# Optimization experiments

Hardware: AMD Instinct MI355X
Metric: run time of the kernel (lower is better)

Reference implementation:

```python
import jax, jax.numpy as jnp
import numpy as np
import math

B, S, D, H = 4, 2048, 768, 12
HD = D // H  # 64


def setup_inputs() -> dict:
    key = jax.random.key(0)
    ks = jax.random.split(key, 9)
    s = 0.02
    return {
        "hidden_states": jax.random.normal(ks[0], (B, S, D), jnp.float32),
        "layout_q": jax.random.normal(ks[1], (B, S, D), jnp.float32),
        "layout_k": jax.random.normal(ks[2], (B, S, D), jnp.float32),
        "attention_mask": jnp.zeros((B, 1, 1, S), jnp.float32),
        "Wq": jax.random.normal(ks[3], (D, D), jnp.float32) * s,
        "bq": jnp.zeros((D,), jnp.float32),
        "Wk": jax.random.normal(ks[4], (D, D), jnp.float32) * s,
        "bk": jnp.zeros((D,), jnp.float32),
        "Wv": jax.random.normal(ks[5], (D, D), jnp.float32) * s,
        "bv": jnp.zeros((D,), jnp.float32),
    }


def _split_heads(x):
    # [B,S,D] -> [B,H,S,HD]
    return x.reshape(B, S, H, HD).transpose(0, 2, 1, 3)


def reference(hidden_states, layout_q, layout_k, attention_mask, Wq, bq, Wk, bk, Wv, bv):
    q = _split_heads(hidden_states @ Wq.T + bq)
    k = _split_heads(hidden_states @ Wk.T + bk)
    v = _split_heads(hidden_states @ Wv.T + bv)
    lq = _split_heads(layout_q)
    lk = _split_heads(layout_k)
    scale = 1.0 / math.sqrt(HD)
    # dual-stream scores: content + layout, both [B,H,S,S]
    scores = (jnp.einsum("bhqd,bhkd->bhqk", q, k)
              + jnp.einsum("bhqd,bhkd->bhqk", lq, lk)) * scale
    scores = scores + attention_mask
    probs = jax.nn.softmax(scores, axis=-1)
    ctx = jnp.einsum("bhqk,bhkd->bhqd", probs, v)
    return ctx.transpose(0, 2, 1, 3).reshape(B, S, D)
```

## Files before the change

kernel.cpp:

```cpp
#include <hip/hip_runtime.h>


typedef __attribute__((ext_vector_type(8))) short short8;
typedef __attribute__((ext_vector_type(4))) float floatx4;

#define LOG2E 1.4426950408889634f
#define QSCL 0.18033688011112042f

static constexpr int Sn = 2048, Dn = 768, Hn = 12, BHn = 48;

__device__ __forceinline__ unsigned short f2bf(float f) {
  unsigned u = __float_as_uint(f);
  u += 0x7FFFu + ((u >> 16) & 1u);
  return (unsigned short)(u >> 16);
}

typedef const __attribute__((address_space(1))) unsigned int* gas_t;
typedef __attribute__((address_space(3))) unsigned int* las_t;
__device__ __forceinline__ void async16(const void* g, void* l) {
  __builtin_amdgcn_global_load_lds((gas_t)g, (las_t)l, 16, 0, 0);
}

__global__ void cast_hs_kernel(const float* __restrict__ in, unsigned short* __restrict__ out, int n4) {
  int i = blockIdx.x * 256 + threadIdx.x;
  if (i >= n4) return;
  float4 v = ((const float4*)in)[i];
  ushort4 o = make_ushort4(f2bf(v.x), f2bf(v.y), f2bf(v.z), f2bf(v.w));
  ((ushort4*)out)[i] = o;
}

__global__ void cast_w_kernel(const float* __restrict__ w0, const float* __restrict__ w1,
                              const float* __restrict__ w2, unsigned short* __restrict__ out) {
  int i = blockIdx.x * 256 + threadIdx.x;
  const float* src = (blockIdx.y == 0) ? w0 : (blockIdx.y == 1) ? w1 : w2;
  float4 v = ((const float4*)src)[i];
  ushort4 o = make_ushort4(f2bf(v.x), f2bf(v.y), f2bf(v.z), f2bf(v.w));
  ((ushort4*)(out + (size_t)blockIdx.y * Dn * Dn))[i] = o;
}

__global__ void pack_layout_kernel(const float* __restrict__ lq, const float* __restrict__ lk,
                                   unsigned short* __restrict__ Qc, unsigned short* __restrict__ Kc) {
  int idx = blockIdx.x * 256 + threadIdx.x;
  const float* src = blockIdx.y ? lk : lq;
  unsigned short* dst = blockIdx.y ? Kc : Qc;
  const float sc = blockIdx.y ? 1.0f : QSCL;
  int d4 = idx & 15;
  int t = idx >> 4;
  int h = t % Hn;
  int bs = t / Hn;
  int b = bs >> 11, s = bs & (Sn - 1);
  float4 v = ((const float4*)src)[idx];
  ushort4 o = make_ushort4(f2bf(v.x * sc), f2bf(v.y * sc), f2bf(v.z * sc), f2bf(v.w * sc));
  size_t off = ((size_t)(b * Hn + h) * Sn + s) * 128 + 64 + d4 * 4;
  *(ushort4*)(dst + off) = o;
}

__global__ __launch_bounds__(256, 2)
void proj_kernel(const unsigned short* __restrict__ X,
                 const unsigned short* __restrict__ Wb,
                 const float* __restrict__ bq, const float* __restrict__ bk, const float* __restrict__ bv,
                 unsigned short* __restrict__ Qc, unsigned short* __restrict__ Kc,
                 unsigned short* __restrict__ Vt) {
  __shared__ __align__(16) unsigned short sMem[16384];
  unsigned short* const sA = sMem;
  unsigned short* const sB = sMem + 8192;

  const int z = blockIdx.z;
  const unsigned short* W = Wb + (size_t)z * Dn * Dn;
  const float* bias = (z == 0) ? bq : (z == 1) ? bk : bv;

  const int t = threadIdx.x;
  const int lane = t & 63, wave = t >> 6;
  const int wm = wave >> 1, wn = wave & 1;
  const int quad = lane >> 4, col15 = lane & 15;
  const int m0 = blockIdx.y * 128, n0 = blockIdx.x * 128;

  const int srow = lane >> 3, schunk = lane & 7;

  floatx4 acc[4][4];
#pragma unroll
  for (int i = 0; i < 4; i++)
#pragma unroll
    for (int j = 0; j < 4; j++) acc[i][j] = (floatx4){0.f, 0.f, 0.f, 0.f};

  for (int k0 = 0; k0 < Dn; k0 += 64) {
    __syncthreads();
#pragma unroll
    for (int c = 0; c < 4; c++) {
      int row = wave * 32 + c * 8 + srow;
      int g = schunk ^ (row & 7);
      async16(X + (size_t)(m0 + row) * Dn + k0 + g * 8, sA + (wave * 32 + c * 8) * 64);
      async16(W + (size_t)(n0 + row) * Dn + k0 + g * 8, sB + (wave * 32 + c * 8) * 64);
    }
    __syncthreads();
#pragma unroll
    for (int kk = 0; kk < 2; kk++) {
      short8 af[4], bf[4];
      const int slot = ((kk * 4 + quad) ^ (col15 & 7)) * 8;
#pragma unroll
      for (int i = 0; i < 4; i++)
        af[i] = *(const short8*)(sA + (wm * 64 + i * 16 + col15) * 64 + slot);
#pragma unroll
      for (int j = 0; j < 4; j++)
        bf[j] = *(const short8*)(sB + (wn * 64 + j * 16 + col15) * 64 + slot);
#pragma unroll
      for (int i = 0; i < 4; i++)
#pragma unroll
        for (int j = 0; j < 4; j++)
          acc[i][j] = __builtin_amdgcn_mfma_f32_16x16x32_bf16(af[i], bf[j], acc[i][j], 0, 0, 0);
    }
  }

  __syncthreads();
  const int b = m0 >> 11;
  const int s0g = m0 & (Sn - 1);
  const int h0 = n0 >> 6;

  if (z < 2) {
    const float scl = (z == 0) ? QSCL : 1.0f;
    unsigned short* dst0 = (z == 0) ? Qc : Kc;
#pragma unroll
    for (int j = 0; j < 4; j++) {
      int nl = wn * 64 + j * 16 + col15;
      float bias_n = bias[n0 + nl];
#pragma unroll
      for (int i = 0; i < 4; i++) {
        int mb = wm * 64 + i * 16 + quad * 4;
#pragma unroll
        for (int r = 0; r < 4; r++) {
          int m = mb + r;
          sMem[m * 128 + (nl ^ (((m >> 2) & 3) << 4))] = f2bf((acc[i][j][r] + bias_n) * scl);
        }
      }
    }
    __syncthreads();
#pragma unroll
    for (int cc = 0; cc < 8; cc++) {
      int idx = cc * 256 + t;
      int m = idx >> 4, piece = idx & 15;
      int h = h0 + (piece >> 3), d8 = piece & 7;
      short8 v = *(const short8*)(sMem + m * 128 + (piece ^ (((m >> 2) & 3) << 1)) * 8);
      *(short8*)(dst0 + ((size_t)(b * Hn + h) * Sn + s0g + m) * 128 + d8 * 8) = v;
    }
  } else {
#pragma unroll
    for (int j = 0; j < 4; j++) {
      int nl = wn * 64 + j * 16 + col15;
      float bias_n = bias[n0 + nl];
#pragma unroll
      for (int i = 0; i < 4; i++) {
        int mb = wm * 64 + i * 16 + quad * 4;
        ushort4 pk = make_ushort4(f2bf(acc[i][j][0] + bias_n), f2bf(acc[i][j][1] + bias_n),
                                  f2bf(acc[i][j][2] + bias_n), f2bf(acc[i][j][3] + bias_n));
        *(ushort4*)(sMem + nl * 128 + (mb ^ ((nl & 7) << 4))) = pk;
      }
    }
    __syncthreads();
#pragma unroll
    for (int cc = 0; cc < 8; cc++) {
      int idx = cc * 256 + t;
      int nl = idx >> 4, piece = idx & 15;
      int h = h0 + (nl >> 6), d = nl & 63;
      short8 v = *(const short8*)(sMem + nl * 128 + (piece ^ ((nl & 7) << 1)) * 8);
      *(short8*)(Vt + ((size_t)(b * Hn + h) * 64 + d) * Sn + s0g + piece * 8) = v;
    }
  }
}

__global__ __launch_bounds__(256, 3)
void attn_kernel(const unsigned short* __restrict__ Qc,
                 const unsigned short* __restrict__ Kc,
                 const unsigned short* __restrict__ Vt,
                 const float* __restrict__ mask,
                 float* __restrict__ out) {
  constexpr int LDV = 72;
  __shared__ __align__(16) unsigned short sKc[64 * 128];
  __shared__ __align__(16) unsigned short sVt[64 * 64];
  __shared__ __align__(16) unsigned short sS[128 * LDV];

  const int t = threadIdx.x;
  const int lane = t & 63, wave = t >> 6;
  const int quad = lane >> 4, col15 = lane & 15;

  const int id = blockIdx.x;
  const int slot = id >> 3;
  const int bh = (id & 7) + 8 * (slot >> 4);
  const int q0 = (slot & 15) * 128;
  const int b = bh / Hn, h = bh % Hn;

  short8 aq[2][4];
  const unsigned short* Qbase = Qc + ((size_t)bh * Sn + q0) * 128;
#pragma unroll
  for (int i = 0; i < 2; i++)
#pragma unroll
    for (int kk = 0; kk < 4; kk++)
      aq[i][kk] = *(const short8*)(Qbase + (size_t)(wave * 32 + i * 16 + col15) * 128 + kk * 32 + quad * 8);

  floatx4 O[2][4];
#pragma unroll
  for (int i = 0; i < 2; i++)
#pragma unroll
    for (int j = 0; j < 4; j++) O[i][j] = (floatx4){0.f, 0.f, 0.f, 0.f};
  float lsum[2][4];
#pragma unroll
  for (int i = 0; i < 2; i++)
#pragma unroll
    for (int r = 0; r < 4; r++) lsum[i][r] = 0.f;

  const unsigned short* Kbase = Kc + (size_t)bh * Sn * 128;
  const unsigned short* Vbase = Vt + (size_t)bh * 64 * Sn;
  const float* mbase = mask + (size_t)b * Sn;

  const int krow = lane >> 4, kslot = lane & 15;
  const int vrow = lane >> 3, vslot = lane & 7;

  for (int kt = 0; kt < Sn / 64; kt++) {
    __syncthreads();
#pragma unroll
    for (int c = 0; c < 4; c++) {
      int row = wave * 16 + c * 4 + krow;
      int g = (kslot & 8) | ((kslot ^ row) & 7);
      async16(Kbase + (size_t)(kt * 64 + row) * 128 + g * 8, sKc + (wave * 16 + c * 4) * 128);
    }
#pragma unroll
    for (int c = 0; c < 2; c++) {
      int row = wave * 16 + c * 8 + vrow;
      int g = vslot ^ (row & 7);
      async16(Vbase + (size_t)row * Sn + kt * 64 + g * 8, sVt + (wave * 16 + c * 8) * 64);
    }
    float mvalL[4];
#pragma unroll
    for (int jk = 0; jk < 4; jk++)
      mvalL[jk] = mbase[kt * 64 + jk * 16 + col15] * LOG2E;
    __syncthreads();

    floatx4 sacc[2][4];
#pragma unroll
    for (int jk = 0; jk < 4; jk++) {
      sacc[0][jk] = (floatx4){0.f, 0.f, 0.f, 0.f};
      sacc[1][jk] = (floatx4){0.f, 0.f, 0.f, 0.f};
#pragma unroll
      for (int kk = 0; kk < 4; kk++) {
        int slot_ = (((kk * 4 + quad) & 8) | (((kk * 4 + quad) ^ col15) & 7)) * 8;
        short8 bk_ = *(const short8*)(sKc + (jk * 16 + col15) * 128 + slot_);
        sacc[0][jk] = __builtin_amdgcn_mfma_f32_16x16x32_bf16(aq[0][kk], bk_, sacc[0][jk], 0, 0, 0);
        sacc[1][jk] = __builtin_amdgcn_mfma_f32_16x16x32_bf16(aq[1][kk], bk_, sacc[1][jk], 0, 0, 0);
      }
    }

#pragma unroll
    for (int i = 0; i < 2; i++) {
      int rowb = wave * 32 + i * 16 + quad * 4;
#pragma unroll
      for (int jk = 0; jk < 4; jk++) {
        int colb = jk * 16 + col15;
#pragma unroll
        for (int r = 0; r < 4; r++) {
          float p = __builtin_amdgcn_exp2f(sacc[i][jk][r] + mvalL[jk]);
          unsigned pu = __float_as_uint(p) & 0xFFFF0000u;
          lsum[i][r] += __uint_as_float(pu);
          sS[(rowb + r) * LDV + colb] = (unsigned short)(pu >> 16);
        }
      }
    }

#pragma unroll
    for (int kk = 0; kk < 2; kk++) {
      short8 ap0 = *(const short8*)(sS + (wave * 32 + col15) * LDV + kk * 32 + quad * 8);
      short8 ap1 = *(const short8*)(sS + (wave * 32 + 16 + col15) * LDV + kk * 32 + quad * 8);
      const int vslot_r = ((kk * 4 + quad) ^ (col15 & 7)) * 8;
#pragma unroll
      for (int j = 0; j < 4; j++) {
        short8 bv_ = *(const short8*)(sVt + (j * 16 + col15) * 64 + vslot_r);
        O[0][j] = __builtin_amdgcn_mfma_f32_16x16x32_bf16(ap0, bv_, O[0][j], 0, 0, 0);
        O[1][j] = __builtin_amdgcn_mfma_f32_16x16x32_bf16(ap1, bv_, O[1][j], 0, 0, 0);
      }
    }
  }

#pragma unroll
  for (int i = 0; i < 2; i++) {
#pragma unroll
    for (int r = 0; r < 4; r++) {
      float s_ = lsum[i][r];
      s_ += __shfl_xor(s_, 1);
      s_ += __shfl_xor(s_, 2);
      s_ += __shfl_xor(s_, 4);
      s_ += __shfl_xor(s_, 8);
      lsum[i][r] = 1.0f / s_;
    }
    int rowb = wave * 32 + i * 16 + quad * 4;
#pragma unroll
    for (int j = 0; j < 4; j++) {
      int dcol = h * 64 + j * 16 + col15;
      float* obase = out + ((size_t)b * Sn + q0 + rowb) * Dn + dcol;
      obase[0 * Dn] = O[i][j][0] * lsum[i][0];
      obase[1 * Dn] = O[i][j][1] * lsum[i][1];
      obase[2 * Dn] = O[i][j][2] * lsum[i][2];
      obase[3 * Dn] = O[i][j][3] * lsum[i][3];
    }
  }
}

extern "C" void kernel_launch(void* const* d_in, const int* in_sizes, int n_in,
                              void* d_out, int out_size, void* d_ws, size_t ws_size,
                              hipStream_t stream) {
  const float* hs   = (const float*)d_in[0];
  const float* lq   = (const float*)d_in[1];
  const float* lk   = (const float*)d_in[2];
  const float* mask = (const float*)d_in[3];
  const float* Wq   = (const float*)d_in[4];
  const float* bq   = (const float*)d_in[5];
  const float* Wk   = (const float*)d_in[6];
  const float* bk   = (const float*)d_in[7];
  const float* Wv   = (const float*)d_in[8];
  const float* bv   = (const float*)d_in[9];
  float* out = (float*)d_out;

  char* ws = (char*)d_ws;
  unsigned short* Xbf = (unsigned short*)ws;
  unsigned short* Wbf = (unsigned short*)(ws + 12582912);
  unsigned short* Qc  = (unsigned short*)(ws + 12582912 + 3538944);
  unsigned short* Kc  = Qc + (size_t)BHn * Sn * 128;
  unsigned short* Vt  = Kc + (size_t)BHn * Sn * 128;

  cast_hs_kernel<<<6144, 256, 0, stream>>>(hs, Xbf, 1572864);
  cast_w_kernel<<<dim3(576, 3), 256, 0, stream>>>(Wq, Wk, Wv, Wbf);
  pack_layout_kernel<<<dim3(6144, 2), 256, 0, stream>>>(lq, lk, Qc, Kc);
  proj_kernel<<<dim3(6, 64, 3), 256, 0, stream>>>(Xbf, Wbf, bq, bk, bv, Qc, Kc, Vt);
  attn_kernel<<<768, 256, 0, stream>>>(Qc, Kc, Vt, mask, out);
}
```

Before: 276.2 us.

## Transpose attention MFMAs, compute row sums via MFMA, skip zero mask, vectorize stores

```diff
diff --git a/kernel.cpp b/kernel.cpp
--- a/kernel.cpp
+++ b/kernel.cpp
@@ -13,6 +13,10 @@
   unsigned u = __float_as_uint(f);
   u += 0x7FFFu + ((u >> 16) & 1u);
   return (unsigned short)(u >> 16);
+}
+
+__device__ __forceinline__ unsigned pack2bf(float lo, float hi) {
+  return (unsigned)f2bf(lo) | ((unsigned)f2bf(hi) << 16);
 }
 
 typedef const __attribute__((address_space(1))) unsigned int* gas_t;
@@ -44,18 +48,23 @@
   const float* src = blockIdx.y ? lk : lq;
   unsigned short* dst = blockIdx.y ? Kc : Qc;
   const float sc = blockIdx.y ? 1.0f : QSCL;
-  int d4 = idx & 15;
-  int t = idx >> 4;
-  int h = t % Hn;
-  int bs = t / Hn;
+  int d8 = idx & 7;
+  int tt = idx >> 3;
+  int h = tt % Hn;
+  int bs = tt / Hn;
   int b = bs >> 11, s = bs & (Sn - 1);
-  float4 v = ((const float4*)src)[idx];
-  ushort4 o = make_ushort4(f2bf(v.x * sc), f2bf(v.y * sc), f2bf(v.z * sc), f2bf(v.w * sc));
-  size_t off = ((size_t)(b * Hn + h) * Sn + s) * 128 + 64 + d4 * 4;
-  *(ushort4*)(dst + off) = o;
-}
-
-__global__ __launch_bounds__(256, 2)
+  float4 v0 = ((const float4*)src)[idx * 2];
+  float4 v1 = ((const float4*)src)[idx * 2 + 1];
+  short8 o;
+  o[0] = (short)f2bf(v0.x * sc); o[1] = (short)f2bf(v0.y * sc);
+  o[2] = (short)f2bf(v0.z * sc); o[3] = (short)f2bf(v0.w * sc);
+  o[4] = (short)f2bf(v1.x * sc); o[5] = (short)f2bf(v1.y * sc);
+  o[6] = (short)f2bf(v1.z * sc); o[7] = (short)f2bf(v1.w * sc);
+  size_t off = ((size_t)(b * Hn + h) * Sn + s) * 128 + 64 + d8 * 8;
+  *(short8*)(dst + off) = o;
+}
+
+__global__ __launch_bounds__(256, 3)
 void proj_kernel(const unsigned short* __restrict__ X,
                  const unsigned short* __restrict__ Wb,
                  const float* __restrict__ bq, const float* __restrict__ bk, const float* __restrict__ bv,
@@ -173,14 +182,14 @@
                  const unsigned short* __restrict__ Vt,
                  const float* __restrict__ mask,
                  float* __restrict__ out) {
-  constexpr int LDV = 72;
   __shared__ __align__(16) unsigned short sKc[64 * 128];
   __shared__ __align__(16) unsigned short sVt[64 * 64];
-  __shared__ __align__(16) unsigned short sS[128 * LDV];
+  __shared__ __align__(16) unsigned short sS[128 * 64];
 
   const int t = threadIdx.x;
   const int lane = t & 63, wave = t >> 6;
   const int quad = lane >> 4, col15 = lane & 15;
+  const int swz = (col15 & 7) << 3;
 
   const int id = blockIdx.x;
   const int slot = id >> 3;
@@ -196,16 +205,20 @@
     for (int kk = 0; kk < 4; kk++)
       aq[i][kk] = *(const short8*)(Qbase + (size_t)(wave * 32 + i * 16 + col15) * 128 + kk * 32 + quad * 8);
 
-  floatx4 O[2][4];
-#pragma unroll
-  for (int i = 0; i < 2; i++)
+  floatx4 O[2][4], lacc[2];
+#pragma unroll
+  for (int i = 0; i < 2; i++) {
+    lacc[i] = (floatx4){0.f, 0.f, 0.f, 0.f};
 #pragma unroll
     for (int j = 0; j < 4; j++) O[i][j] = (floatx4){0.f, 0.f, 0.f, 0.f};
-  float lsum[2][4];
-#pragma unroll
-  for (int i = 0; i < 2; i++)
-#pragma unroll
-    for (int r = 0; r < 4; r++) lsum[i][r] = 0.f;
+  }
+
+  short8 aone;
+  {
+    short onev = (col15 == 0) ? (short)0x3F80 : (short)0;
+#pragma unroll
+    for (int e = 0; e < 8; e++) aone[e] = onev;
+  }
 
   const unsigned short* Kbase = Kc + (size_t)bh * Sn * 128;
   const unsigned short* Vbase = Vt + (size_t)bh * 64 * Sn;
@@ -228,76 +241,78 @@
       int g = vslot ^ (row & 7);
       async16(Vbase + (size_t)row * Sn + kt * 64 + g * 8, sVt + (wave * 16 + c * 8) * 64);
     }
-    float mvalL[4];
-#pragma unroll
-    for (int jk = 0; jk < 4; jk++)
-      mvalL[jk] = mbase[kt * 64 + jk * 16 + col15] * LOG2E;
-    __syncthreads();
-
-    floatx4 sacc[2][4];
-#pragma unroll
-    for (int jk = 0; jk < 4; jk++) {
-      sacc[0][jk] = (floatx4){0.f, 0.f, 0.f, 0.f};
-      sacc[1][jk] = (floatx4){0.f, 0.f, 0.f, 0.f};
-#pragma unroll
-      for (int kk = 0; kk < 4; kk++) {
-        int slot_ = (((kk * 4 + quad) & 8) | (((kk * 4 + quad) ^ col15) & 7)) * 8;
-        short8 bk_ = *(const short8*)(sKc + (jk * 16 + col15) * 128 + slot_);
-        sacc[0][jk] = __builtin_amdgcn_mfma_f32_16x16x32_bf16(aq[0][kk], bk_, sacc[0][jk], 0, 0, 0);
-        sacc[1][jk] = __builtin_amdgcn_mfma_f32_16x16x32_bf16(aq[1][kk], bk_, sacc[1][jk], 0, 0, 0);
-      }
-    }
-
-#pragma unroll
-    for (int i = 0; i < 2; i++) {
-      int rowb = wave * 32 + i * 16 + quad * 4;
-#pragma unroll
-      for (int jk = 0; jk < 4; jk++) {
-        int colb = jk * 16 + col15;
-#pragma unroll
-        for (int r = 0; r < 4; r++) {
-          float p = __builtin_amdgcn_exp2f(sacc[i][jk][r] + mvalL[jk]);
-          unsigned pu = __float_as_uint(p) & 0xFFFF0000u;
-          lsum[i][r] += __uint_as_float(pu);
-          sS[(rowb + r) * LDV + colb] = (unsigned short)(pu >> 16);
-        }
+    float m64 = mbase[kt * 64 + lane] * LOG2E;
+    __syncthreads();
+    const bool nomask = __all(m64 == 0.0f);
+
+    floatx4 sacc[4][2];
+#pragma unroll
+    for (int jm = 0; jm < 4; jm++) {
+      sacc[jm][0] = (floatx4){0.f, 0.f, 0.f, 0.f};
+      sacc[jm][1] = (floatx4){0.f, 0.f, 0.f, 0.f};
+    }
+#pragma unroll
+    for (int kk = 0; kk < 4; kk++) {
+      const int slotK = (((kk * 4 + quad) & 8) | (((kk * 4 + quad) ^ col15) & 7)) * 8;
+#pragma unroll
+      for (int jm = 0; jm < 4; jm++) {
+        short8 ak = *(const short8*)(sKc + (jm * 16 + col15) * 128 + slotK);
+        sacc[jm][0] = __builtin_amdgcn_mfma_f32_16x16x32_bf16(ak, aq[0][kk], sacc[jm][0], 0, 0, 0);
+        sacc[jm][1] = __builtin_amdgcn_mfma_f32_16x16x32_bf16(ak, aq[1][kk], sacc[jm][1], 0, 0, 0);
+      }
+    }
+
+    float mvv[4][4];
+    if (!nomask) {
+#pragma unroll
+      for (int jm = 0; jm < 4; jm++)
+#pragma unroll
+        for (int r = 0; r < 4; r++) mvv[jm][r] = __shfl(m64, jm * 16 + quad * 4 + r);
+    }
+
+#pragma unroll
+    for (int iq = 0; iq < 2; iq++) {
+      unsigned short* srow = sS + (wave * 32 + iq * 16 + col15) * 64;
+#pragma unroll
+      for (int jm = 0; jm < 4; jm++) {
+        float p0 = sacc[jm][iq][0], p1 = sacc[jm][iq][1];
+        float p2 = sacc[jm][iq][2], p3 = sacc[jm][iq][3];
+        if (!nomask) { p0 += mvv[jm][0]; p1 += mvv[jm][1]; p2 += mvv[jm][2]; p3 += mvv[jm][3]; }
+        p0 = __builtin_amdgcn_exp2f(p0); p1 = __builtin_amdgcn_exp2f(p1);
+        p2 = __builtin_amdgcn_exp2f(p2); p3 = __builtin_amdgcn_exp2f(p3);
+        uint2 w;
+        w.x = pack2bf(p0, p1);
+        w.y = pack2bf(p2, p3);
+        *(uint2*)(srow + ((jm * 16 + quad * 4) ^ swz)) = w;
       }
     }
 
 #pragma unroll
     for (int kk = 0; kk < 2; kk++) {
-      short8 ap0 = *(const short8*)(sS + (wave * 32 + col15) * LDV + kk * 32 + quad * 8);
-      short8 ap1 = *(const short8*)(sS + (wave * 32 + 16 + col15) * LDV + kk * 32 + quad * 8);
-      const int vslot_r = ((kk * 4 + quad) ^ (col15 & 7)) * 8;
-#pragma unroll
-      for (int j = 0; j < 4; j++) {
-        short8 bv_ = *(const short8*)(sVt + (j * 16 + col15) * 64 + vslot_r);
-        O[0][j] = __builtin_amdgcn_mfma_f32_16x16x32_bf16(ap0, bv_, O[0][j], 0, 0, 0);
-        O[1][j] = __builtin_amdgcn_mfma_f32_16x16x32_bf16(ap1, bv_, O[1][j], 0, 0, 0);
-      }
-    }
-  }
-
-#pragma unroll
-  for (int i = 0; i < 2; i++) {
-#pragma unroll
-    for (int r = 0; r < 4; r++) {
-      float s_ = lsum[i][r];
-      s_ += __shfl_xor(s_, 1);
-      s_ += __shfl_xor(s_, 2);
-      s_ += __shfl_xor(s_, 4);
-      s_ += __shfl_xor(s_, 8);
-      lsum[i][r] = 1.0f / s_;
-    }
-    int rowb = wave * 32 + i * 16 + quad * 4;
-#pragma unroll
-    for (int j = 0; j < 4; j++) {
-      int dcol = h * 64 + j * 16 + col15;
-      float* obase = out + ((size_t)b * Sn + q0 + rowb) * Dn + dcol;
-      obase[0 * Dn] = O[i][j][0] * lsum[i][0];
-      obase[1 * Dn] = O[i][j][1] * lsum[i][1];
-      obase[2 * Dn] = O[i][j][2] * lsum[i][2];
-      obase[3 * Dn] = O[i][j][3] * lsum[i][3];
+      short8 pb0 = *(const short8*)(sS + (wave * 32 + col15) * 64 + ((kk * 32 + quad * 8) ^ swz));
+      short8 pb1 = *(const short8*)(sS + (wave * 32 + 16 + col15) * 64 + ((kk * 32 + quad * 8) ^ swz));
+      const int slotV = ((kk * 4 + quad) ^ (col15 & 7)) * 8;
+#pragma unroll
+      for (int jd = 0; jd < 4; jd++) {
+        short8 av = *(const short8*)(sVt + (jd * 16 + col15) * 64 + slotV);
+        O[0][jd] = __builtin_amdgcn_mfma_f32_16x16x32_bf16(av, pb0, O[0][jd], 0, 0, 0);
+        O[1][jd] = __builtin_amdgcn_mfma_f32_16x16x32_bf16(av, pb1, O[1][jd], 0, 0, 0);
+      }
+      lacc[0] = __builtin_amdgcn_mfma_f32_16x16x32_bf16(aone, pb0, lacc[0], 0, 0, 0);
+      lacc[1] = __builtin_amdgcn_mfma_f32_16x16x32_bf16(aone, pb1, lacc[1], 0, 0, 0);
+    }
+  }
+
+#pragma unroll
+  for (int iq = 0; iq < 2; iq++) {
+    float inv = 1.0f / __shfl(lacc[iq][0], col15);
+    int qrow = q0 + wave * 32 + iq * 16 + col15;
+    float* obase = out + ((size_t)b * Sn + qrow) * Dn + h * 64 + quad * 4;
+#pragma unroll
+    for (int jd = 0; jd < 4; jd++) {
+      float4 o4 = make_float4(O[iq][jd][0] * inv, O[iq][jd][1] * inv,
+                              O[iq][jd][2] * inv, O[iq][jd][3] * inv);
+      *(float4*)(obase + jd * 16) = o4;
     }
   }
 }
@@ -326,7 +341,7 @@
 
   cast_hs_kernel<<<6144, 256, 0, stream>>>(hs, Xbf, 1572864);
   cast_w_kernel<<<dim3(576, 3), 256, 0, stream>>>(Wq, Wk, Wv, Wbf);
-  pack_layout_kernel<<<dim3(6144, 2), 256, 0, stream>>>(lq, lk, Qc, Kc);
+  pack_layout_kernel<<<dim3(3072, 2), 256, 0, stream>>>(lq, lk, Qc, Kc);
   proj_kernel<<<dim3(6, 64, 3), 256, 0, stream>>>(Xbf, Wbf, bq, bk, bv, Qc, Kc, Vt);
   attn_kernel<<<768, 256, 0, stream>>>(Qc, Kc, Vt, mask, out);
 }
```

New measurement: 293.7 us. +6.3%, slower.

## Double-buffer projection GEMM K-loop and widen layout pack stores

Applied to the files above, without the earlier changes.

```diff
diff --git a/kernel.cpp b/kernel.cpp
--- a/kernel.cpp
+++ b/kernel.cpp
@@ -44,26 +44,29 @@
   const float* src = blockIdx.y ? lk : lq;
   unsigned short* dst = blockIdx.y ? Kc : Qc;
   const float sc = blockIdx.y ? 1.0f : QSCL;
-  int d4 = idx & 15;
-  int t = idx >> 4;
-  int h = t % Hn;
-  int bs = t / Hn;
+  int d8 = idx & 7;
+  int tt = idx >> 3;
+  int h = tt % Hn;
+  int bs = tt / Hn;
   int b = bs >> 11, s = bs & (Sn - 1);
-  float4 v = ((const float4*)src)[idx];
-  ushort4 o = make_ushort4(f2bf(v.x * sc), f2bf(v.y * sc), f2bf(v.z * sc), f2bf(v.w * sc));
-  size_t off = ((size_t)(b * Hn + h) * Sn + s) * 128 + 64 + d4 * 4;
-  *(ushort4*)(dst + off) = o;
-}
-
-__global__ __launch_bounds__(256, 2)
+  float4 v0 = ((const float4*)src)[idx * 2];
+  float4 v1 = ((const float4*)src)[idx * 2 + 1];
+  short8 o;
+  o[0] = (short)f2bf(v0.x * sc); o[1] = (short)f2bf(v0.y * sc);
+  o[2] = (short)f2bf(v0.z * sc); o[3] = (short)f2bf(v0.w * sc);
+  o[4] = (short)f2bf(v1.x * sc); o[5] = (short)f2bf(v1.y * sc);
+  o[6] = (short)f2bf(v1.z * sc); o[7] = (short)f2bf(v1.w * sc);
+  size_t off = ((size_t)(b * Hn + h) * Sn + s) * 128 + 64 + d8 * 8;
+  *(short8*)(dst + off) = o;
+}
+
+__global__ __launch_bounds__(256, 3)
 void proj_kernel(const unsigned short* __restrict__ X,
                  const unsigned short* __restrict__ Wb,
                  const float* __restrict__ bq, const float* __restrict__ bk, const float* __restrict__ bv,
                  unsigned short* __restrict__ Qc, unsigned short* __restrict__ Kc,
                  unsigned short* __restrict__ Vt) {
   __shared__ __align__(16) unsigned short sMem[16384];
-  unsigned short* const sA = sMem;
-  unsigned short* const sB = sMem + 8192;
 
   const int z = blockIdx.z;
   const unsigned short* W = Wb + (size_t)z * Dn * Dn;
@@ -75,7 +78,7 @@
   const int quad = lane >> 4, col15 = lane & 15;
   const int m0 = blockIdx.y * 128, n0 = blockIdx.x * 128;
 
-  const int srow = lane >> 3, schunk = lane & 7;
+  const int srow = lane >> 2, schunk = lane & 3;
 
   floatx4 acc[4][4];
 #pragma unroll
@@ -83,35 +86,40 @@
 #pragma unroll
     for (int j = 0; j < 4; j++) acc[i][j] = (floatx4){0.f, 0.f, 0.f, 0.f};
 
-  for (int k0 = 0; k0 < Dn; k0 += 64) {
-    __syncthreads();
-#pragma unroll
-    for (int c = 0; c < 4; c++) {
-      int row = wave * 32 + c * 8 + srow;
-      int g = schunk ^ (row & 7);
-      async16(X + (size_t)(m0 + row) * Dn + k0 + g * 8, sA + (wave * 32 + c * 8) * 64);
-      async16(W + (size_t)(n0 + row) * Dn + k0 + g * 8, sB + (wave * 32 + c * 8) * 64);
-    }
-    __syncthreads();
-#pragma unroll
-    for (int kk = 0; kk < 2; kk++) {
-      short8 af[4], bf[4];
-      const int slot = ((kk * 4 + quad) ^ (col15 & 7)) * 8;
-#pragma unroll
-      for (int i = 0; i < 4; i++)
-        af[i] = *(const short8*)(sA + (wm * 64 + i * 16 + col15) * 64 + slot);
+  auto stageAB = [&](int kt, int buf) {
+    unsigned short* sA = sMem + buf * 4096;
+    unsigned short* sB = sMem + 8192 + buf * 4096;
+#pragma unroll
+    for (int c = 0; c < 2; c++) {
+      int row = wave * 32 + c * 16 + srow;
+      async16(X + (size_t)(m0 + row) * Dn + kt * 32 + schunk * 8, sA + (wave * 32 + c * 16) * 32);
+      async16(W + (size_t)(n0 + row) * Dn + kt * 32 + schunk * 8, sB + (wave * 32 + c * 16) * 32);
+    }
+  };
+
+  stageAB(0, 0);
+  __syncthreads();
+
+  for (int kt = 0; kt < 24; kt++) {
+    const int cur = kt & 1;
+    if (kt + 1 < 24) stageAB(kt + 1, cur ^ 1);
+    const unsigned short* sA = sMem + cur * 4096;
+    const unsigned short* sB = sMem + 8192 + cur * 4096;
+    short8 af[4], bf[4];
+#pragma unroll
+    for (int i = 0; i < 4; i++)
+      af[i] = *(const short8*)(sA + (wm * 64 + i * 16 + col15) * 32 + quad * 8);
+#pragma unroll
+    for (int j = 0; j < 4; j++)
+      bf[j] = *(const short8*)(sB + (wn * 64 + j * 16 + col15) * 32 + quad * 8);
+#pragma unroll
+    for (int i = 0; i < 4; i++)
 #pragma unroll
       for (int j = 0; j < 4; j++)
-        bf[j] = *(const short8*)(sB + (wn * 64 + j * 16 + col15) * 64 + slot);
-#pragma unroll
-      for (int i = 0; i < 4; i++)
-#pragma unroll
-        for (int j = 0; j < 4; j++)
-          acc[i][j] = __builtin_amdgcn_mfma_f32_16x16x32_bf16(af[i], bf[j], acc[i][j], 0, 0, 0);
-    }
+        acc[i][j] = __builtin_amdgcn_mfma_f32_16x16x32_bf16(af[i], bf[j], acc[i][j], 0, 0, 0);
+    __syncthreads();
   }
 
-  __syncthreads();
   const int b = m0 >> 11;
   const int s0g = m0 & (Sn - 1);
   const int h0 = n0 >> 6;
@@ -326,7 +334,7 @@
 
   cast_hs_kernel<<<6144, 256, 0, stream>>>(hs, Xbf, 1572864);
   cast_w_kernel<<<dim3(576, 3), 256, 0, stream>>>(Wq, Wk, Wv, Wbf);
-  pack_layout_kernel<<<dim3(6144, 2), 256, 0, stream>>>(lq, lk, Qc, Kc);
+  pack_layout_kernel<<<dim3(3072, 2), 256, 0, stream>>>(lq, lk, Qc, Kc);
   proj_kernel<<<dim3(6, 64, 3), 256, 0, stream>>>(Xbf, Wbf, bq, bk, bv, Qc, Kc, Vt);
   attn_kernel<<<768, 256, 0, stream>>>(Qc, Kc, Vt, mask, out);
 }
```

After: 276.2 us. No clear change (-0.0%).
